# Performance work log

Hardware: AMD Instinct MI355X
Metric: run time of the kernel (lower is better)

## Reference

```python
import jax, jax.numpy as jnp
import numpy as np

B, S = 16, 32            # batch, cfg.feature_samples
CF, CC, H, W = 768, 512, 28, 28
NEG = 2                  # cfg.neg_samples
POS_INTRA_SHIFT, POS_INTER_SHIFT, NEG_INTER_SHIFT = 0.18, 0.12, 0.46


def _norm(t):
    # F.normalize(t, dim=1, eps=1e-10)
    n = jnp.sqrt(jnp.sum(t * t, axis=1, keepdims=True))
    return t / jnp.maximum(n, 1e-10)


def _grid_sample(img, grid):
    # torch F.grid_sample, bilinear, padding_mode='border', align_corners=True
    # img [B,C,H,W], grid [B,Hg,Wg,2] with (x,y) in [-1,1]
    Hh, Ww = img.shape[2], img.shape[3]
    x = (grid[..., 0] + 1.0) * 0.5 * (Ww - 1)
    y = (grid[..., 1] + 1.0) * 0.5 * (Hh - 1)
    x0 = jnp.floor(x); y0 = jnp.floor(y)
    wx = x - x0; wy = y - y0
    x0c = jnp.clip(x0, 0, Ww - 1).astype(jnp.int32)
    x1c = jnp.clip(x0 + 1, 0, Ww - 1).astype(jnp.int32)
    y0c = jnp.clip(y0, 0, Hh - 1).astype(jnp.int32)
    y1c = jnp.clip(y0 + 1, 0, Hh - 1).astype(jnp.int32)
    gather = jax.vmap(lambda im, yy, xx: im[:, yy, xx])  # -> [B,C,Hg,Wg]
    Ia, Ib = gather(img, y0c, x0c), gather(img, y1c, x0c)
    Ic, Id = gather(img, y0c, x1c), gather(img, y1c, x1c)
    wx = wx[:, None]; wy = wy[:, None]
    return Ia * (1 - wx) * (1 - wy) + Ib * (1 - wx) * wy + Ic * wx * (1 - wy) + Id * wx * wy


def _sample(t, coords):
    # sample(): grid_sample(t, coords.permute(0,2,1,3))
    return _grid_sample(t, jnp.transpose(coords, (0, 2, 1, 3)))


def _corr(a, b):
    return jnp.einsum('nchw,ncij->nhwij', a, b)


def _helper(f1, f2, c1, c2, shift):
    # fd computed under no_grad in torch
    fd = jax.lax.stop_gradient(_corr(_norm(f1), _norm(f2)))
    # cfg.pointwise = True
    old_mean = fd.mean()
    fd = fd - fd.mean(axis=(3, 4), keepdims=True)
    fd = fd - fd.mean() + old_mean
    cd = _corr(_norm(c1), _norm(c2))
    # cfg.zero_clamp=True, cfg.stabalize=False -> cd.clamp(0.0)
    return -jnp.maximum(cd, 0.0) * (fd - shift)


def setup_inputs() -> dict:
    key = jax.random.key(0)
    ks = jax.random.split(key, 11)
    return {
        'orig_feats': jax.random.normal(ks[0], (B, CF, H, W), jnp.float32),
        'orig_feats_pos': jax.random.normal(ks[1], (B, CF, H, W), jnp.float32),
        'orig_salience': jax.random.uniform(ks[2], (B, 224, 224), jnp.float32),
        'orig_salience_pos': jax.random.uniform(ks[3], (B, 224, 224), jnp.float32),
        'orig_code': jax.random.normal(ks[4], (B, CC, H, W), jnp.float32),
        'orig_code_pos': jax.random.normal(ks[5], (B, CC, H, W), jnp.float32),
        'depth': jax.random.uniform(ks[6], (B, 1, 224, 224), jnp.float32),
        'depth_pos': jax.random.uniform(ks[7], (B, 1, 224, 224), jnp.float32),
        'coords1': jax.random.uniform(ks[8], (B, S, S, 2), jnp.float32),
        'coords2': jax.random.uniform(ks[9], (B, S, S, 2), jnp.float32),
        'perms': jax.random.randint(ks[10], (NEG, B), 0, B, jnp.int32),
    }


def reference(orig_feats, orig_feats_pos, orig_salience, orig_salience_pos,
              orig_code, orig_code_pos, depth, depth_pos,
              coords1, coords2, perms):
    # random-coordinate branch: coords = rand(...) * 2 - 1
    c1 = coords1 * 2.0 - 1.0
    c2 = coords2 * 2.0 - 1.0
    feats = _sample(orig_feats, c1)
    code = _sample(orig_code, c1)
    feats_pos = _sample(orig_feats_pos, c2)
    code_pos = _sample(orig_code_pos, c2)

    pos_intra = _helper(feats, feats, code, code, POS_INTRA_SHIFT).mean()
    pos_inter = _helper(feats, feats_pos, code, code_pos, POS_INTER_SHIFT).mean()

    def neg_one(perm):
        feats_neg = _sample(orig_feats[perm], c2)
        code_neg = _sample(orig_code[perm], c2)
        return _helper(feats, feats_neg, code, code_neg, NEG_INTER_SHIFT).mean()

    neg_inter = jax.vmap(neg_one)(perms).mean()
    return jnp.stack([pos_intra, pos_inter, neg_inter])
```

## Files before the change

kernel.cpp:

```cpp
#include <hip/hip_runtime.h>
#include <hip/hip_bf16.h>

#define NB 16
#define NP 1024
#define CF 768
#define CC 512
#define HH 28
#define WW 28
#define HW 784
#define NTOT 16777216.0f

typedef short bf16x8 __attribute__((ext_vector_type(8)));
typedef float f32x4 __attribute__((ext_vector_type(4)));
struct __align__(8) bf4 { __hip_bfloat16 a, b, c, d; };

__device__ __forceinline__ float b2f(__hip_bfloat16 h) { return __bfloat162float(h); }


__global__ void transpose_bf16_kernel(const float* __restrict__ in0,
                                      const float* __restrict__ in1,
                                      __hip_bfloat16* __restrict__ out, int C) {
  __shared__ float tile[32][33];
  int p0 = blockIdx.x * 32, c0 = blockIdx.y * 32;
  int t = blockIdx.z >> 4, b = blockIdx.z & 15;
  int tx = threadIdx.x, ty = threadIdx.y;
  const float* ib = (t == 0 ? in0 : in1) + (size_t)b * C * HW;
  __hip_bfloat16* ob = out + ((size_t)t * NB + b) * HW * C;
#pragma unroll
  for (int i = 0; i < 32; i += 8) {
    int c = c0 + ty + i, p = p0 + tx;
    if (p < HW) tile[ty + i][tx] = ib[(size_t)c * HW + p];
  }
  __syncthreads();
#pragma unroll
  for (int i = 0; i < 32; i += 8) {
    int p = p0 + ty + i, c = c0 + tx;
    if (p < HW) ob[(size_t)p * C + c] = __float2bfloat16(tile[tx][ty + i]);
  }
}

__global__ __launch_bounds__(256) void sample_pack_kernel(
    const __hip_bfloat16* __restrict__ fTb, const __hip_bfloat16* __restrict__ cTb,
    const float* __restrict__ coords1, const float* __restrict__ coords2,
    const int* __restrict__ perms,
    __hip_bfloat16* __restrict__ Fb, __hip_bfloat16* __restrict__ Cb,
    float* __restrict__ scF, float* __restrict__ scC) {
  __shared__ int offs[4][64];
  __shared__ float wts[4][64];
  __shared__ char tile[8320];

  int bb = blockIdx.y, slot = blockIdx.z;
  int tid = threadIdx.x;
  int p0 = blockIdx.x * 64;
  int pt = blockIdx.x >> 1, mh = blockIdx.x & 1;

  const float* coords = (slot == 0) ? coords1 : coords2;
  int srcidx;
  if (slot == 0)      srcidx = bb;
  else if (slot == 1) srcidx = 16 + bb;
  else if (slot == 2) srcidx = perms[bb];
  else                srcidx = perms[16 + bb];

  if (tid < 64) {
    int p = p0 + tid;
    float cx = coords[((size_t)bb * NP + p) * 2 + 0];
    float cy = coords[((size_t)bb * NP + p) * 2 + 1];
    float x = cx * (WW - 1), y = cy * (HH - 1);
    float x0f = floorf(x), y0f = floorf(y);
    float wx = x - x0f, wy = y - y0f;
    int x0 = min(max((int)x0f, 0), WW - 1);
    int x1 = min(max((int)x0f + 1, 0), WW - 1);
    int y0 = min(max((int)y0f, 0), HH - 1);
    int y1 = min(max((int)y0f + 1, 0), HH - 1);
    offs[0][tid] = y0 * WW + x0;
    offs[1][tid] = y1 * WW + x0;
    offs[2][tid] = y0 * WW + x1;
    offs[3][tid] = y1 * WW + x1;
    wts[0][tid] = (1.f - wx) * (1.f - wy);
    wts[1][tid] = (1.f - wx) * wy;
    wts[2][tid] = wx * (1.f - wy);
    wts[3][tid] = wx * wy;
  }
  __syncthreads();

  int gid = tid >> 4, l = tid & 15;
  int r = l >> 1, half = l & 1;

  {
    const __hip_bfloat16* base = fTb + (size_t)srcidx * HW * CF;
    float ssq[4] = {0.f, 0.f, 0.f, 0.f};
    for (int kt = 0; kt < 12; ++kt) {
#pragma unroll
      for (int j = 0; j < 4; ++j) {
        int m = j * 16 + gid;
        float4 v = {0.f, 0.f, 0.f, 0.f};
#pragma unroll
        for (int c = 0; c < 4; ++c) {
          const bf4 t4 = *((const bf4*)(base + (size_t)offs[c][m] * CF) + kt * 16 + l);
          float wv = wts[c][m];
          v.x += wv * b2f(t4.a); v.y += wv * b2f(t4.b);
          v.z += wv * b2f(t4.c); v.w += wv * b2f(t4.d);
        }
        ssq[j] += v.x * v.x + v.y * v.y + v.z * v.z + v.w * v.w;
        bf4 o = {__float2bfloat16(v.x), __float2bfloat16(v.y),
                 __float2bfloat16(v.z), __float2bfloat16(v.w)};
        int cl = r * 64 + m;
        *(bf4*)(tile + cl * 16 + r * 16 + half * 8) = o;
      }
      __syncthreads();
      char* gbase = (char*)Fb +
          (((((size_t)slot * NB + bb) * 12 + kt) * 8 + pt) * 1024 + (size_t)mh * 64) * 16;
#pragma unroll
      for (int jj = 0; jj < 2; ++jj) {
        int cl = jj * 256 + tid;
        int rr = cl >> 6, mi = cl & 63;
        float4 val = *(const float4*)(tile + cl * 16 + rr * 16);
        *(float4*)(gbase + (size_t)(rr * 128 + mi) * 16) = val;
      }
      __syncthreads();
    }
#pragma unroll
    for (int j = 0; j < 4; ++j) {
#pragma unroll
      for (int mm = 1; mm < 16; mm <<= 1) ssq[j] += __shfl_xor(ssq[j], mm);
    }
    if (l == 0) {
#pragma unroll
      for (int j = 0; j < 4; ++j) {
        int p = p0 + j * 16 + gid;
        scF[((size_t)slot * NB + bb) * NP + p] = 1.f / fmaxf(sqrtf(ssq[j]), 1e-10f);
      }
    }
  }

  {
    const __hip_bfloat16* base = cTb + (size_t)srcidx * HW * CC;
    float ssq[4] = {0.f, 0.f, 0.f, 0.f};
    for (int kt = 0; kt < 8; ++kt) {
#pragma unroll
      for (int j = 0; j < 4; ++j) {
        int m = j * 16 + gid;
        float4 v = {0.f, 0.f, 0.f, 0.f};
#pragma unroll
        for (int c = 0; c < 4; ++c) {
          const bf4 t4 = *((const bf4*)(base + (size_t)offs[c][m] * CC) + kt * 16 + l);
          float wv = wts[c][m];
          v.x += wv * b2f(t4.a); v.y += wv * b2f(t4.b);
          v.z += wv * b2f(t4.c); v.w += wv * b2f(t4.d);
        }
        ssq[j] += v.x * v.x + v.y * v.y + v.z * v.z + v.w * v.w;
        bf4 o = {__float2bfloat16(v.x), __float2bfloat16(v.y),
                 __float2bfloat16(v.z), __float2bfloat16(v.w)};
        int cl = r * 64 + m;
        *(bf4*)(tile + cl * 16 + r * 16 + half * 8) = o;
      }
      __syncthreads();
      char* gbase = (char*)Cb +
          (((((size_t)slot * NB + bb) * 8 + kt) * 8 + pt) * 1024 + (size_t)mh * 64) * 16;
#pragma unroll
      for (int jj = 0; jj < 2; ++jj) {
        int cl = jj * 256 + tid;
        int rr = cl >> 6, mi = cl & 63;
        float4 val = *(const float4*)(tile + cl * 16 + rr * 16);
        *(float4*)(gbase + (size_t)(rr * 128 + mi) * 16) = val;
      }
      __syncthreads();
    }
#pragma unroll
    for (int j = 0; j < 4; ++j) {
#pragma unroll
      for (int mm = 1; mm < 16; mm <<= 1) ssq[j] += __shfl_xor(ssq[j], mm);
    }
    if (l == 0) {
#pragma unroll
      for (int j = 0; j < 4; ++j) {
        int p = p0 + j * 16 + gid;
        scC[((size_t)slot * NB + bb) * NP + p] = 1.f / fmaxf(sqrtf(ssq[j]), 1e-10f);
      }
    }
  }
}

__device__ __forceinline__ void stage_sup(const __hip_bfloat16* __restrict__ st,
                                          bf16x8* buf, int tid) {
#pragma unroll
  for (int i = 0; i < 4; ++i) {
    const __hip_bfloat16* g = st + (size_t)(i * 256 + tid) * 8;
    __builtin_amdgcn_global_load_lds(
        (const __attribute__((address_space(1))) void*)g,
        (__attribute__((address_space(3))) void*)&buf[i * 256 + (tid & 192)],
        16, 0, 0);
  }
}

__global__ __launch_bounds__(256, 2) void corr_kernel(
    const __hip_bfloat16* __restrict__ Fb, const __hip_bfloat16* __restrict__ Cb,
    const float* __restrict__ scF, const float* __restrict__ scC,
    float* __restrict__ rowfd, float* __restrict__ rowrcd,
    float* __restrict__ cross) {
  __shared__ bf16x8 Afs[1024], Bfs[1024], Acs[1024], Bcs[1024];

  int id = blockIdx.x;
  int zl = id & 7, q = id >> 3;
  int bx = q & 7, by = (q >> 3) & 7, zh = q >> 6;
  int z = zh * 8 + zl;
  int h = z >> 4, bb = z & 15;
  int p0 = bx * 128, q0 = by * 128;
  int tid = threadIdx.x, ln = tid & 63, w = tid >> 6;
  int wm = w >> 1, wn = w & 1, quad = ln >> 4, t16 = ln & 15;

  const __hip_bfloat16* AfB = Fb + (((size_t)bb * 12) * 8 + bx) * 8192;
  const __hip_bfloat16* BfB = Fb + ((((size_t)h * NB + bb) * 12) * 8 + by) * 8192;
  const __hip_bfloat16* AcB = Cb + (((size_t)bb * 8) * 8 + bx) * 8192;
  const __hip_bfloat16* BcB = Cb + ((((size_t)h * NB + bb) * 8) * 8 + by) * 8192;
  const size_t KTSTR = (size_t)8 * 8192;

  f32x4 accf[4][4], accc[4][4];
#pragma unroll
  for (int i = 0; i < 4; ++i)
#pragma unroll
    for (int j = 0; j < 4; ++j) {
      accf[i][j] = (f32x4){0.f, 0.f, 0.f, 0.f};
      accc[i][j] = (f32x4){0.f, 0.f, 0.f, 0.f};
    }

  for (int kt = 0; kt < 12; ++kt) {
    stage_sup(AfB + kt * KTSTR, Afs, tid);
    stage_sup(BfB + kt * KTSTR, Bfs, tid);
    if (kt < 8) {
      stage_sup(AcB + kt * KTSTR, Acs, tid);
      stage_sup(BcB + kt * KTSTR, Bcs, tid);
    }
    __syncthreads();
#pragma unroll
    for (int s = 0; s < 2; ++s) {
      bf16x8 a[4], b[4];
#pragma unroll
      for (int mi = 0; mi < 4; ++mi)
        a[mi] = Afs[s * 512 + quad * 128 + wm * 64 + mi * 16 + t16];
#pragma unroll
      for (int ni = 0; ni < 4; ++ni)
        b[ni] = Bfs[s * 512 + quad * 128 + wn * 64 + ni * 16 + t16];
#pragma unroll
      for (int mi = 0; mi < 4; ++mi)
#pragma unroll
        for (int ni = 0; ni < 4; ++ni)
          accf[mi][ni] = __builtin_amdgcn_mfma_f32_16x16x32_bf16(
              a[mi], b[ni], accf[mi][ni], 0, 0, 0);
    }
    if (kt < 8) {
#pragma unroll
      for (int s = 0; s < 2; ++s) {
        bf16x8 a[4], b[4];
#pragma unroll
        for (int mi = 0; mi < 4; ++mi)
          a[mi] = Acs[s * 512 + quad * 128 + wm * 64 + mi * 16 + t16];
#pragma unroll
        for (int ni = 0; ni < 4; ++ni)
          b[ni] = Bcs[s * 512 + quad * 128 + wn * 64 + ni * 16 + t16];
#pragma unroll
        for (int mi = 0; mi < 4; ++mi)
#pragma unroll
          for (int ni = 0; ni < 4; ++ni)
            accc[mi][ni] = __builtin_amdgcn_mfma_f32_16x16x32_bf16(
                a[mi], b[ni], accc[mi][ni], 0, 0, 0);
      }
    }
    __syncthreads();
  }

  float* sm = (float*)Afs;
  {
    const float* s0 = scF + (size_t)bb * NP;
    const float* s1 = scF + ((size_t)h * NB + bb) * NP;
    const float* s2 = scC + (size_t)bb * NP;
    const float* s3 = scC + ((size_t)h * NB + bb) * NP;
    if (tid < 128) {
      sm[tid] = s0[p0 + tid];
      sm[256 + tid] = s2[p0 + tid];
    } else {
      int u = tid - 128;
      sm[128 + u] = s1[q0 + u];
      sm[384 + u] = s3[q0 + u];
    }
  }
  __syncthreads();

  float sbf[4], sbc[4];
#pragma unroll
  for (int ni = 0; ni < 4; ++ni) {
    int qq = wn * 64 + ni * 16 + t16;
    sbf[ni] = sm[128 + qq];
    sbc[ni] = sm[384 + qq];
  }
  float cross_l = 0.f;
#pragma unroll
  for (int mi = 0; mi < 4; ++mi) {
#pragma unroll
    for (int r = 0; r < 4; ++r) {
      int pl = wm * 64 + mi * 16 + quad * 4 + r;
      float saf = sm[pl], sac = sm[256 + pl];
      float sfd = 0.f, srw = 0.f;
#pragma unroll
      for (int ni = 0; ni < 4; ++ni) {
        float fd = accf[mi][ni][r] * (saf * sbf[ni]);
        float cd = accc[mi][ni][r] * (sac * sbc[ni]);
        float rc = fmaxf(cd, 0.f);
        sfd += fd;
        srw += rc;
        cross_l += rc * fd;
      }
#pragma unroll
      for (int mm = 1; mm < 16; mm <<= 1) {
        sfd += __shfl_xor(sfd, mm);
        srw += __shfl_xor(srw, mm);
      }
      if (t16 == 0) {
        int p = p0 + pl;
        size_t idx = ((size_t)h * NB + bb) * NP + p;
        atomicAdd(&rowfd[idx], sfd);
        atomicAdd(&rowrcd[idx], srw);
      }
    }
  }
#pragma unroll
  for (int mm = 1; mm < 64; mm <<= 1) cross_l += __shfl_xor(cross_l, mm);
  float* crs = (float*)Bfs;
  if (ln == 0) crs[w] = cross_l;
  __syncthreads();
  if (tid == 0) atomicAdd(&cross[h], crs[0] + crs[1] + crs[2] + crs[3]);
}

__global__ void finalize_partial(const float* __restrict__ rowfd,
                                 const float* __restrict__ rowrcd,
                                 const float* __restrict__ cross,
                                 float* __restrict__ losses) {
  __shared__ float r1[16], r2[16], r3[16];
  const float shifts[4] = {0.18f, 0.12f, 0.46f, 0.46f};
  int h = blockIdx.x, tid = threadIdx.x, w = tid >> 6, ln = tid & 63;
  float s1 = 0.f, s2 = 0.f, s3 = 0.f;
  for (int i = tid; i < NB * NP; i += 1024) {
    float a = rowfd[h * NB * NP + i];
    float c = rowrcd[h * NB * NP + i];
    s1 += a;
    s2 += c;
    s3 += a * c;
  }
#pragma unroll
  for (int mm = 1; mm < 64; mm <<= 1) {
    s1 += __shfl_xor(s1, mm);
    s2 += __shfl_xor(s2, mm);
    s3 += __shfl_xor(s3, mm);
  }
  if (ln == 0) { r1[w] = s1; r2[w] = s2; r3[w] = s3; }
  __syncthreads();
  if (tid == 0) {
    float Sfd = 0.f, Srcd = 0.f, Sdot = 0.f;
#pragma unroll
    for (int i = 0; i < 16; ++i) { Sfd += r1[i]; Srcd += r2[i]; Sdot += r3[i]; }
    losses[h] = -(cross[h] - Sdot * (1.0f / 1024.0f) +
                  (Sfd / NTOT - shifts[h]) * Srcd) / NTOT;
  }
}

__global__ void finalize_combine(const float* __restrict__ losses,
                                 float* __restrict__ out) {
  if (threadIdx.x == 0) {
    out[0] = losses[0];
    out[1] = losses[1];
    out[2] = 0.5f * (losses[2] + losses[3]);
  }
}

extern "C" void kernel_launch(void* const* d_in, const int* in_sizes, int n_in,
                              void* d_out, int out_size, void* d_ws, size_t ws_size,
                              hipStream_t stream) {
  (void)in_sizes; (void)n_in; (void)out_size; (void)ws_size;
  const float* orig_feats = (const float*)d_in[0];
  const float* orig_feats_pos = (const float*)d_in[1];
  const float* orig_code = (const float*)d_in[4];
  const float* orig_code_pos = (const float*)d_in[5];
  const float* coords1 = (const float*)d_in[8];
  const float* coords2 = (const float*)d_in[9];
  const int* perms = (const int*)d_in[10];
  float* out = (float*)d_out;

  char* ws = (char*)d_ws;
  size_t off = 0;
  __hip_bfloat16* fTb = (__hip_bfloat16*)(ws + off); off += (size_t)2 * NB * HW * CF * 2;
  __hip_bfloat16* cTb = (__hip_bfloat16*)(ws + off); off += (size_t)2 * NB * HW * CC * 2;
  __hip_bfloat16* Fb = (__hip_bfloat16*)(ws + off); off += (size_t)4 * NB * NP * CF * 2;
  __hip_bfloat16* Cb = (__hip_bfloat16*)(ws + off); off += (size_t)4 * NB * NP * CC * 2;
  float* rowfd  = (float*)(ws + off); off += (size_t)4 * NB * NP * 4;
  float* rowrcd = (float*)(ws + off); off += (size_t)4 * NB * NP * 4;
  float* cross  = (float*)(ws + off); off += 64;
  float* losses = (float*)(ws + off); off += 64;
  float* scF    = (float*)(ws + off); off += (size_t)4 * NB * NP * 4;
  float* scC    = (float*)(ws + off); off += (size_t)4 * NB * NP * 4;

  (void)hipMemsetAsync(rowfd, 0, (size_t)4 * NB * NP * 4 * 2 + 128, stream);

  dim3 tb(32, 8);
  transpose_bf16_kernel<<<dim3(25, 24, 32), tb, 0, stream>>>(
      orig_feats, orig_feats_pos, fTb, CF);
  transpose_bf16_kernel<<<dim3(25, 16, 32), tb, 0, stream>>>(
      orig_code, orig_code_pos, cTb, CC);
  sample_pack_kernel<<<dim3(16, 16, 4), 256, 0, stream>>>(
      fTb, cTb, coords1, coords2, perms, Fb, Cb, scF, scC);

  corr_kernel<<<dim3(4096), 256, 0, stream>>>(Fb, Cb, scF, scC,
                                              rowfd, rowrcd, cross);
  finalize_partial<<<4, 1024, 0, stream>>>(rowfd, rowrcd, cross, losses);
  finalize_combine<<<1, 64, 0, stream>>>(losses, out);
}
```

Baseline: 482.1 us.

## Pack sampled features as fp8 and use fp8 MFMA for correlations

The sampled feature and code matrices are now quantized to fp8 (unscaled, before normalization) instead of bf16, and the correlation kernel uses the fp8 16x16x32 MFMA instead of the bf16 one. This halves the packed operand memory and LDS traffic and uses the higher-throughput fp8 matrix path. Unnormalized values with no scaling risk large precision loss or saturation in fp8 e4m3, which may push results past the tolerance.

Result: faster. 417.6 us (-13.4%).

```diff
diff --git a/kernel.cpp b/kernel.cpp
--- a/kernel.cpp
+++ b/kernel.cpp
@@ -10,7 +10,6 @@
 #define HW 784
 #define NTOT 16777216.0f
 
-typedef short bf16x8 __attribute__((ext_vector_type(8)));
 typedef float f32x4 __attribute__((ext_vector_type(4)));
 struct __align__(8) bf4 { __hip_bfloat16 a, b, c, d; };
 
@@ -43,11 +42,11 @@
     const __hip_bfloat16* __restrict__ fTb, const __hip_bfloat16* __restrict__ cTb,
     const float* __restrict__ coords1, const float* __restrict__ coords2,
     const int* __restrict__ perms,
-    __hip_bfloat16* __restrict__ Fb, __hip_bfloat16* __restrict__ Cb,
+    unsigned char* __restrict__ Fb, unsigned char* __restrict__ Cb,
     float* __restrict__ scF, float* __restrict__ scC) {
   __shared__ int offs[4][64];
   __shared__ float wts[4][64];
-  __shared__ char tile[8320];
+  __shared__ char tile[4160];
 
   int bb = blockIdx.y, slot = blockIdx.z;
   int tid = threadIdx.x;
@@ -84,7 +83,7 @@
   __syncthreads();
 
   int gid = tid >> 4, l = tid & 15;
-  int r = l >> 1, half = l & 1;
+  int r = l >> 1, h4 = l & 1;
 
   {
     const __hip_bfloat16* base = fTb + (size_t)srcidx * HW * CF;
@@ -102,20 +101,19 @@
           v.z += wv * b2f(t4.c); v.w += wv * b2f(t4.d);
         }
         ssq[j] += v.x * v.x + v.y * v.y + v.z * v.z + v.w * v.w;
-        bf4 o = {__float2bfloat16(v.x), __float2bfloat16(v.y),
-                 __float2bfloat16(v.z), __float2bfloat16(v.w)};
-        int cl = r * 64 + m;
-        *(bf4*)(tile + cl * 16 + r * 16 + half * 8) = o;
+        int w0 = __builtin_amdgcn_cvt_pk_fp8_f32(v.x, v.y, 0, false);
+        int w1 = __builtin_amdgcn_cvt_pk_fp8_f32(v.z, v.w, w0, true);
+        *(int*)(tile + r * 520 + m * 8 + h4 * 4) = w1;
       }
       __syncthreads();
-      char* gbase = (char*)Fb +
-          (((((size_t)slot * NB + bb) * 12 + kt) * 8 + pt) * 1024 + (size_t)mh * 64) * 16;
+      unsigned char* gbase = Fb +
+          (((((size_t)slot * NB + bb) * 12 + kt) * 8 + pt) * 1024 + (size_t)mh * 64) * 8;
 #pragma unroll
       for (int jj = 0; jj < 2; ++jj) {
         int cl = jj * 256 + tid;
         int rr = cl >> 6, mi = cl & 63;
-        float4 val = *(const float4*)(tile + cl * 16 + rr * 16);
-        *(float4*)(gbase + (size_t)(rr * 128 + mi) * 16) = val;
+        unsigned long long val = *(const unsigned long long*)(tile + rr * 520 + mi * 8);
+        *(unsigned long long*)(gbase + (size_t)(rr * 128 + mi) * 8) = val;
       }
       __syncthreads();
     }
@@ -149,20 +147,19 @@
           v.z += wv * b2f(t4.c); v.w += wv * b2f(t4.d);
         }
         ssq[j] += v.x * v.x + v.y * v.y + v.z * v.z + v.w * v.w;
-        bf4 o = {__float2bfloat16(v.x), __float2bfloat16(v.y),
-                 __float2bfloat16(v.z), __float2bfloat16(v.w)};
-        int cl = r * 64 + m;
-        *(bf4*)(tile + cl * 16 + r * 16 + half * 8) = o;
+        int w0 = __builtin_amdgcn_cvt_pk_fp8_f32(v.x, v.y, 0, false);
+        int w1 = __builtin_amdgcn_cvt_pk_fp8_f32(v.z, v.w, w0, true);
+        *(int*)(tile + r * 520 + m * 8 + h4 * 4) = w1;
       }
       __syncthreads();
-      char* gbase = (char*)Cb +
-          (((((size_t)slot * NB + bb) * 8 + kt) * 8 + pt) * 1024 + (size_t)mh * 64) * 16;
+      unsigned char* gbase = Cb +
+          (((((size_t)slot * NB + bb) * 8 + kt) * 8 + pt) * 1024 + (size_t)mh * 64) * 8;
 #pragma unroll
       for (int jj = 0; jj < 2; ++jj) {
         int cl = jj * 256 + tid;
         int rr = cl >> 6, mi = cl & 63;
-        float4 val = *(const float4*)(tile + cl * 16 + rr * 16);
-        *(float4*)(gbase + (size_t)(rr * 128 + mi) * 16) = val;
+        unsigned long long val = *(const unsigned long long*)(tile + rr * 520 + mi * 8);
+        *(unsigned long long*)(gbase + (size_t)(rr * 128 + mi) * 8) = val;
       }
       __syncthreads();
     }
@@ -181,24 +178,25 @@
   }
 }
 
-__device__ __forceinline__ void stage_sup(const __hip_bfloat16* __restrict__ st,
-                                          bf16x8* buf, int tid) {
-#pragma unroll
-  for (int i = 0; i < 4; ++i) {
-    const __hip_bfloat16* g = st + (size_t)(i * 256 + tid) * 8;
+__device__ __forceinline__ void stage_sup(const unsigned long long* __restrict__ st,
+                                          unsigned long long* buf, int tid) {
+#pragma unroll
+  for (int i = 0; i < 2; ++i) {
+    const char* g = (const char*)st + (size_t)(i * 256 + tid) * 16;
+    char* d = (char*)buf + i * 4096 + (tid & 192) * 16;
     __builtin_amdgcn_global_load_lds(
         (const __attribute__((address_space(1))) void*)g,
-        (__attribute__((address_space(3))) void*)&buf[i * 256 + (tid & 192)],
-        16, 0, 0);
+        (__attribute__((address_space(3))) void*)d, 16, 0, 0);
   }
 }
 
 __global__ __launch_bounds__(256, 2) void corr_kernel(
-    const __hip_bfloat16* __restrict__ Fb, const __hip_bfloat16* __restrict__ Cb,
+    const unsigned long long* __restrict__ Fb,
+    const unsigned long long* __restrict__ Cb,
     const float* __restrict__ scF, const float* __restrict__ scC,
     float* __restrict__ rowfd, float* __restrict__ rowrcd,
     float* __restrict__ cross) {
-  __shared__ bf16x8 Afs[1024], Bfs[1024], Acs[1024], Bcs[1024];
+  __shared__ unsigned long long Afs[1024], Bfs[1024], Acs[1024], Bcs[1024];
 
   int id = blockIdx.x;
   int zl = id & 7, q = id >> 3;
@@ -209,11 +207,11 @@
   int tid = threadIdx.x, ln = tid & 63, w = tid >> 6;
   int wm = w >> 1, wn = w & 1, quad = ln >> 4, t16 = ln & 15;
 
-  const __hip_bfloat16* AfB = Fb + (((size_t)bb * 12) * 8 + bx) * 8192;
-  const __hip_bfloat16* BfB = Fb + ((((size_t)h * NB + bb) * 12) * 8 + by) * 8192;
-  const __hip_bfloat16* AcB = Cb + (((size_t)bb * 8) * 8 + bx) * 8192;
-  const __hip_bfloat16* BcB = Cb + ((((size_t)h * NB + bb) * 8) * 8 + by) * 8192;
-  const size_t KTSTR = (size_t)8 * 8192;
+  const unsigned long long* AfB = Fb + (((size_t)bb * 12) * 8 + bx) * 1024;
+  const unsigned long long* BfB = Fb + ((((size_t)h * NB + bb) * 12) * 8 + by) * 1024;
+  const unsigned long long* AcB = Cb + (((size_t)bb * 8) * 8 + bx) * 1024;
+  const unsigned long long* BcB = Cb + ((((size_t)h * NB + bb) * 8) * 8 + by) * 1024;
+  const size_t KTSTR = (size_t)8 * 1024;
 
   f32x4 accf[4][4], accc[4][4];
 #pragma unroll
@@ -234,35 +232,35 @@
     __syncthreads();
 #pragma unroll
     for (int s = 0; s < 2; ++s) {
-      bf16x8 a[4], b[4];
+      long a[4], b[4];
 #pragma unroll
       for (int mi = 0; mi < 4; ++mi)
-        a[mi] = Afs[s * 512 + quad * 128 + wm * 64 + mi * 16 + t16];
+        a[mi] = (long)Afs[s * 512 + quad * 128 + wm * 64 + mi * 16 + t16];
 #pragma unroll
       for (int ni = 0; ni < 4; ++ni)
-        b[ni] = Bfs[s * 512 + quad * 128 + wn * 64 + ni * 16 + t16];
+        b[ni] = (long)Bfs[s * 512 + quad * 128 + wn * 64 + ni * 16 + t16];
 #pragma unroll
       for (int mi = 0; mi < 4; ++mi)
 #pragma unroll
         for (int ni = 0; ni < 4; ++ni)
-          accf[mi][ni] = __builtin_amdgcn_mfma_f32_16x16x32_bf16(
+          accf[mi][ni] = __builtin_amdgcn_mfma_f32_16x16x32_fp8_fp8(
               a[mi], b[ni], accf[mi][ni], 0, 0, 0);
     }
     if (kt < 8) {
 #pragma unroll
       for (int s = 0; s < 2; ++s) {
-        bf16x8 a[4], b[4];
+        long a[4], b[4];
 #pragma unroll
         for (int mi = 0; mi < 4; ++mi)
-          a[mi] = Acs[s * 512 + quad * 128 + wm * 64 + mi * 16 + t16];
+          a[mi] = (long)Acs[s * 512 + quad * 128 + wm * 64 + mi * 16 + t16];
 #pragma unroll
         for (int ni = 0; ni < 4; ++ni)
-          b[ni] = Bcs[s * 512 + quad * 128 + wn * 64 + ni * 16 + t16];
+          b[ni] = (long)Bcs[s * 512 + quad * 128 + wn * 64 + ni * 16 + t16];
 #pragma unroll
         for (int mi = 0; mi < 4; ++mi)
 #pragma unroll
           for (int ni = 0; ni < 4; ++ni)
-            accc[mi][ni] = __builtin_amdgcn_mfma_f32_16x16x32_bf16(
+            accc[mi][ni] = __builtin_amdgcn_mfma_f32_16x16x32_fp8_fp8(
                 a[mi], b[ni], accc[mi][ni], 0, 0, 0);
       }
     }
@@ -389,8 +387,8 @@
   size_t off = 0;
   __hip_bfloat16* fTb = (__hip_bfloat16*)(ws + off); off += (size_t)2 * NB * HW * CF * 2;
   __hip_bfloat16* cTb = (__hip_bfloat16*)(ws + off); off += (size_t)2 * NB * HW * CC * 2;
-  __hip_bfloat16* Fb = (__hip_bfloat16*)(ws + off); off += (size_t)4 * NB * NP * CF * 2;
-  __hip_bfloat16* Cb = (__hip_bfloat16*)(ws + off); off += (size_t)4 * NB * NP * CC * 2;
+  unsigned char* Fb = (unsigned char*)(ws + off); off += (size_t)4 * NB * NP * CF;
+  unsigned char* Cb = (unsigned char*)(ws + off); off += (size_t)4 * NB * NP * CC;
   float* rowfd  = (float*)(ws + off); off += (size_t)4 * NB * NP * 4;
   float* rowrcd = (float*)(ws + off); off += (size_t)4 * NB * NP * 4;
   float* cross  = (float*)(ws + off); off += 64;
@@ -408,8 +406,9 @@
   sample_pack_kernel<<<dim3(16, 16, 4), 256, 0, stream>>>(
       fTb, cTb, coords1, coords2, perms, Fb, Cb, scF, scC);
 
-  corr_kernel<<<dim3(4096), 256, 0, stream>>>(Fb, Cb, scF, scC,
-                                              rowfd, rowrcd, cross);
+  corr_kernel<<<dim3(4096), 256, 0, stream>>>(
+      (const unsigned long long*)Fb, (const unsigned long long*)Cb,
+      scF, scC, rowfd, rowrcd, cross);
   finalize_partial<<<4, 1024, 0, stream>>>(rowfd, rowrcd, cross, losses);
   finalize_combine<<<1, 64, 0, stream>>>(losses, out);
 }
```
